# Kernel tuning notes

Hardware: AMD Instinct MI355X
Metric: run time of the kernel (lower is better)

Reference implementation:

```python
import jax, jax.numpy as jnp
import numpy as np

B, S, I, H, O, E, K = 2, 2048, 4096, 1376, 4096, 8, 2
BALANCE_W = 0.01  # balance_loss_weight in llama-moe


def setup_inputs() -> dict:
    key = jax.random.key(0)
    ks = jax.random.split(key, 6)
    sc = lambda k, shape, fan: jax.random.normal(k, shape, jnp.float32) * (fan ** -0.5)
    return {
        "x": jax.random.normal(ks[0], (B, S, I), jnp.float32),
        "gate_w": sc(ks[1], (E, I), I),          # linear gate network, no bias
        "w_gate": sc(ks[2], (E, H, I), I),       # GLU gate proj per expert
        "b_gate": jnp.zeros((E, H), jnp.float32),
        "w_up": sc(ks[3], (E, H, I), I),         # GLU up proj per expert
        "b_up": jnp.zeros((E, H), jnp.float32),
        "w_down": sc(ks[4], (E, O, H), H),       # down proj per expert
        "b_down": jnp.zeros((E, O), jnp.float32),
    }


def _cv_squared(v, eps=1e-10):
    # torch: x.var() / (x.mean()**2 + eps), unbiased variance
    mean = jnp.mean(v)
    var = jnp.sum((v - mean) ** 2) / (v.shape[0] - 1)
    return var / (mean ** 2 + eps)


def reference(x, gate_w, w_gate, b_gate, w_up, b_up, w_down, b_down):
    bsz, seq, _ = x.shape
    xt = x.reshape(-1, I)                         # [T, I] tokens
    T = xt.shape[0]

    # ---- TopKBalancedNoisyGate (no-noise branch) ----
    logits = xt @ gate_w.T                        # [T, E]
    top_logits, top_idx = jax.lax.top_k(logits, K)
    top_scores = jax.nn.softmax(top_logits, axis=-1)   # softmax over top-k logits
    # dense routing matrix: zeros.scatter(1, top_idx, top_scores)
    dense = jnp.zeros((T, E), xt.dtype).at[jnp.arange(T)[:, None], top_idx].set(top_scores)
    importance = dense.sum(axis=0)                # [E]
    load = (dense > 0).astype(jnp.float32).sum(axis=0)  # [E]
    gate_loss = BALANCE_W * (_cv_squared(importance) + _cv_squared(load))

    # ---- UniversalCalculator over LinearGLUExperts ----
    # Dense-dispatch formulation: compute every expert on every token, weight by
    # the (mostly-zero) routing matrix -> identical math to gather/grouped-GEMM/scatter.
    g = jnp.einsum('ti,ehi->teh', xt, w_gate) + b_gate        # [T, E, H]
    u = jnp.einsum('ti,ehi->teh', xt, w_up) + b_up            # [T, E, H]
    inter = jax.nn.silu(g) * u                                # GLU
    # score * (W_down h + b_down) == W_down (score*h) + score*b_down
    y = jnp.einsum('teh,eoh->to', inter * dense[:, :, None], w_down) + dense @ b_down
    return y.reshape(bsz, seq, O), gate_loss
```

## Files before the change

### kernel.cpp

```cpp
#include <hip/hip_runtime.h>
#include <hip/hip_bf16.h>
#include <stdint.h>

#define TN 4096
#define DI 4096
#define DH 1376
#define DHP 1408
#define DO 4096
#define NE 8
#define NPAIR 8192

typedef unsigned short u16;
typedef __bf16 bf16x8 __attribute__((ext_vector_type(8)));
typedef float f32x4 __attribute__((ext_vector_type(4)));
typedef uint32_t u32x4 __attribute__((ext_vector_type(4)));

__device__ __forceinline__ uint32_t pack2bf(float a, float b) {
    union { float f; uint32_t u; } ua, ub;
    ua.f = a; ub.f = b;
    uint32_t lo = (ua.u + 0x7fffu + ((ua.u >> 16) & 1u)) >> 16;
    uint32_t hi = (ub.u + 0x7fffu + ((ub.u >> 16) & 1u)) >> 16;
    return lo | (hi << 16);
}
__device__ __forceinline__ u16 f2bf(float a) {
    union { float f; uint32_t u; } ua; ua.f = a;
    return (u16)((ua.u + 0x7fffu + ((ua.u >> 16) & 1u)) >> 16);
}
__device__ __forceinline__ void gload16(const void* g, void* l) {
    __builtin_amdgcn_global_load_lds(
        (const __attribute__((address_space(1))) void*)g,
        (__attribute__((address_space(3))) void*)l, 16, 0, 0);
}

__global__ __launch_bounds__(256) void k_cvt(const float* __restrict__ src,
                                             u16* __restrict__ dst, int n8)
{
    int i = blockIdx.x * 256 + threadIdx.x;
    if (i >= n8) return;
    const float4* s = (const float4*)(src + (size_t)i * 8);
    float4 a = s[0], b = s[1];
    u32x4 q = {pack2bf(a.x, a.y), pack2bf(a.z, a.w), pack2bf(b.x, b.y), pack2bf(b.z, b.w)};
    *(u32x4*)(dst + (size_t)i * 8) = q;
}

__global__ __launch_bounds__(256) void k_cvt_wd(const float* __restrict__ src,
                                                u16* __restrict__ dst)
{
    int i = blockIdx.x * 256 + threadIdx.x;
    int row = i / 176, c8 = (i % 176) * 8;
    u32x4 q = {0u, 0u, 0u, 0u};
    if (c8 < DH) {
        const float4* s = (const float4*)(src + (size_t)row * DH + c8);
        float4 a = s[0], b = s[1];
        q = (u32x4){pack2bf(a.x, a.y), pack2bf(a.z, a.w), pack2bf(b.x, b.y), pack2bf(b.z, b.w)};
    }
    *(u32x4*)(dst + (size_t)row * DHP + c8) = q;
}

__global__ __launch_bounds__(256) void k_gate(
    const float* __restrict__ x, const float* __restrict__ gw,
    u16* __restrict__ x16, int* __restrict__ tke, float* __restrict__ tks,
    int* __restrict__ cnt, float* __restrict__ imp)
{
    int t = blockIdx.x, tid = threadIdx.x;
    const float* xr = x + (size_t)t * DI;
    double acc[NE];
#pragma unroll
    for (int e = 0; e < NE; ++e) acc[e] = 0.0;
#pragma unroll
    for (int j = 0; j < 4; ++j) {
        int i4 = (j * 256 + tid) * 4;
        float4 xv = *(const float4*)(xr + i4);
        uint2 p; p.x = pack2bf(xv.x, xv.y); p.y = pack2bf(xv.z, xv.w);
        *(uint2*)(x16 + (size_t)t * DI + i4) = p;
#pragma unroll
        for (int e = 0; e < NE; ++e) {
            float4 wv = *(const float4*)(gw + (size_t)e * DI + i4);
            acc[e] = fma((double)xv.x, (double)wv.x, acc[e]);
            acc[e] = fma((double)xv.y, (double)wv.y, acc[e]);
            acc[e] = fma((double)xv.z, (double)wv.z, acc[e]);
            acc[e] = fma((double)xv.w, (double)wv.w, acc[e]);
        }
    }
#pragma unroll
    for (int o = 32; o > 0; o >>= 1)
#pragma unroll
        for (int e = 0; e < NE; ++e) acc[e] += __shfl_down(acc[e], o, 64);
    __shared__ double lred[4][NE];
    if ((tid & 63) == 0)
#pragma unroll
        for (int e = 0; e < NE; ++e) lred[tid >> 6][e] = acc[e];
    __syncthreads();
    if (tid == 0) {
        double lg[NE];
#pragma unroll
        for (int e = 0; e < NE; ++e) lg[e] = lred[0][e] + lred[1][e] + lred[2][e] + lred[3][e];
        int e1 = 0;
        for (int e = 1; e < NE; ++e) if (lg[e] > lg[e1]) e1 = e;
        int e2 = -1;
        for (int e = 0; e < NE; ++e) { if (e == e1) continue; if (e2 < 0 || lg[e] > lg[e2]) e2 = e; }
        float d = (float)(lg[e2] - lg[e1]);
        float ed = expf(d);
        float s1 = 1.0f / (1.0f + ed);
        float s2 = ed / (1.0f + ed);
        tke[2 * t] = e1; tke[2 * t + 1] = e2;
        tks[2 * t] = s1; tks[2 * t + 1] = s2;
        atomicAdd(&cnt[e1], 1); atomicAdd(&cnt[e2], 1);
        unsafeAtomicAdd(&imp[e1], s1); unsafeAtomicAdd(&imp[e2], s2);
    }
}

__global__ void k_finalize(const int* __restrict__ cnt, const float* __restrict__ imp,
                           int* __restrict__ off, float* __restrict__ loss_out)
{
    if (threadIdx.x == 0 && blockIdx.x == 0) {
        int o = 0;
        for (int e = 0; e < NE; ++e) { off[e] = o; o += cnt[e]; }
        float m1 = 0.f, m2 = 0.f;
        for (int e = 0; e < NE; ++e) { m1 += imp[e]; m2 += (float)cnt[e]; }
        m1 *= 0.125f; m2 *= 0.125f;
        float v1 = 0.f, v2 = 0.f;
        for (int e = 0; e < NE; ++e) {
            float d1 = imp[e] - m1, d2 = (float)cnt[e] - m2;
            v1 += d1 * d1; v2 += d2 * d2;
        }
        v1 /= 7.0f; v2 /= 7.0f;
        float cv1 = v1 / (m1 * m1 + 1e-10f);
        float cv2 = v2 / (m2 * m2 + 1e-10f);
        *loss_out = 0.01f * (cv1 + cv2);
    }
}

__global__ __launch_bounds__(256) void k_scatter(
    const int* __restrict__ tke, const float* __restrict__ tks,
    const int* __restrict__ off, int* __restrict__ fill,
    int* __restrict__ tok, float* __restrict__ sc)
{
    int t = blockIdx.x * 256 + threadIdx.x;
    if (t >= TN) return;
#pragma unroll
    for (int k = 0; k < 2; ++k) {
        int e = tke[2 * t + k];
        int pos = off[e] + atomicAdd(&fill[e], 1);
        tok[pos] = t; sc[pos] = tks[2 * t + k];
    }
}

__global__ __launch_bounds__(256) void k_yinit(
    const int* __restrict__ tke, const float* __restrict__ tks,
    const float* __restrict__ bd, float* __restrict__ y)
{
    int t = blockIdx.x, tid = threadIdx.x;
    int e1 = tke[2 * t], e2 = tke[2 * t + 1];
    float s1 = tks[2 * t], s2 = tks[2 * t + 1];
    const float4* b1 = (const float4*)(bd + (size_t)e1 * DO);
    const float4* b2 = (const float4*)(bd + (size_t)e2 * DO);
    float4* yr = (float4*)(y + (size_t)t * DO);
#pragma unroll
    for (int j = 0; j < 4; ++j) {
        int i = j * 256 + tid;
        float4 a = b1[i], b = b2[i], r;
        r.x = s1 * a.x + s2 * b.x; r.y = s1 * a.y + s2 * b.y;
        r.z = s1 * a.z + s2 * b.z; r.w = s1 * a.w + s2 * b.w;
        yr[i] = r;
    }
}


__global__ __launch_bounds__(256, 2) void k_stage1b(
    const u16* __restrict__ x16,
    const u16* __restrict__ wg16, const u16* __restrict__ wu16,
    const float* __restrict__ bg, const float* __restrict__ bu,
    const int* __restrict__ cnt, const int* __restrict__ off,
    const int* __restrict__ tok, const float* __restrict__ sc,
    u16* __restrict__ inter)
{
    int e = blockIdx.x & 7;
    int ce = cnt[e];
    int rows0 = (blockIdx.x >> 3) * 128;
    if (rows0 >= ce) return;
    int oe = off[e];
    int h0 = blockIdx.y * 128;
    int tid = threadIdx.x;

    __shared__ u16 As[128 * 64];
    __shared__ u16 Gs[128 * 64];
    __shared__ u16 Us[128 * 64];

    int swzc = ((tid & 7) ^ ((tid >> 3) & 7)) * 8;
    const u16* abase[4]; const u16* gbase[4]; const u16* ubase[4];
#pragma unroll
    for (int i = 0; i < 4; ++i) {
        int rl = i * 32 + (tid >> 3);
        int rg = oe + min(rows0 + rl, ce - 1);
        abase[i] = x16 + (size_t)tok[rg] * DI + swzc;
        int hr = min(h0 + rl, DH - 1);
        gbase[i] = wg16 + ((size_t)e * DH + hr) * DI + swzc;
        ubase[i] = wu16 + ((size_t)e * DH + hr) * DI + swzc;
    }
    int wid = tid >> 6, lane = tid & 63;

    f32x4 accg[4][4], accu[4][4];
    f32x4 vz = {0.f, 0.f, 0.f, 0.f};
#pragma unroll
    for (int m = 0; m < 4; ++m)
#pragma unroll
        for (int n = 0; n < 4; ++n) { accg[m][n] = vz; accu[m][n] = vz; }

    int wm = wid >> 1, wn = wid & 1;
    int rA = wm * 64 + (lane & 15);
    int rB = wn * 64 + (lane & 15);
    int quarter = lane >> 4;
    int swzr = lane & 7;

    for (int k0 = 0; k0 < DI; k0 += 64) {
#pragma unroll
        for (int i = 0; i < 4; ++i) {
            gload16(abase[i] + k0, &As[i * 2048 + wid * 512]);
            gload16(gbase[i] + k0, &Gs[i * 2048 + wid * 512]);
            gload16(ubase[i] + k0, &Us[i * 2048 + wid * 512]);
        }
        __syncthreads();
#pragma unroll
        for (int kk = 0; kk < 2; ++kk) {
            int cb = ((kk * 4 + quarter) ^ swzr) * 8;
            bf16x8 a[4], g[4], u[4];
#pragma unroll
            for (int m = 0; m < 4; ++m)
                a[m] = *(const bf16x8*)&As[(rA + m * 16) * 64 + cb];
#pragma unroll
            for (int n = 0; n < 4; ++n) {
                g[n] = *(const bf16x8*)&Gs[(rB + n * 16) * 64 + cb];
                u[n] = *(const bf16x8*)&Us[(rB + n * 16) * 64 + cb];
            }
#pragma unroll
            for (int m = 0; m < 4; ++m)
#pragma unroll
                for (int n = 0; n < 4; ++n) {
                    accg[m][n] = __builtin_amdgcn_mfma_f32_16x16x32_bf16(a[m], g[n], accg[m][n], 0, 0, 0);
                    accu[m][n] = __builtin_amdgcn_mfma_f32_16x16x32_bf16(a[m], u[n], accu[m][n], 0, 0, 0);
                }
        }
        __syncthreads();
    }

    int rmax = ce - rows0;
    float bgv[4], buv[4];
    int hc[4]; bool hok[4];
#pragma unroll
    for (int n = 0; n < 4; ++n) {
        hc[n] = h0 + wn * 64 + n * 16 + (lane & 15);
        hok[n] = hc[n] < DH;
        bgv[n] = hok[n] ? bg[e * DH + hc[n]] : 0.f;
        buv[n] = hok[n] ? bu[e * DH + hc[n]] : 0.f;
    }
#pragma unroll
    for (int m = 0; m < 4; ++m) {
#pragma unroll
        for (int r = 0; r < 4; ++r) {
            int rl = wm * 64 + m * 16 + (lane >> 4) * 4 + r;
            if (rl < rmax) {
                int rg = oe + rows0 + rl;
                float s = sc[rg];
                size_t rowb = (size_t)rg * DHP;
#pragma unroll
                for (int n = 0; n < 4; ++n) {
                    float v = 0.f;
                    if (hok[n]) {
                        float gv = accg[m][n][r] + bgv[n];
                        float uv = accu[m][n][r] + buv[n];
                        float sig = 1.0f / (1.0f + __expf(-gv));
                        v = s * gv * sig * uv;
                    }
                    inter[rowb + hc[n]] = f2bf(v);
                }
            }
        }
    }
}

__global__ __launch_bounds__(256, 2) void k_stage2b(
    const u16* __restrict__ inter, const u16* __restrict__ wd16,
    const int* __restrict__ cnt, const int* __restrict__ off,
    const int* __restrict__ tok, float* __restrict__ y)
{
    int e = blockIdx.x & 7;
    int ce = cnt[e];
    int rows0 = (blockIdx.x >> 3) * 128;
    if (rows0 >= ce) return;
    int oe = off[e];
    int o0 = blockIdx.y * 128;
    int tid = threadIdx.x;

    __shared__ u16 As[128 * 64];
    __shared__ u16 Bs[128 * 64];

    int swzc = ((tid & 7) ^ ((tid >> 3) & 7)) * 8;
    const u16* abase[4]; const u16* bbase[4];
#pragma unroll
    for (int i = 0; i < 4; ++i) {
        int rl = i * 32 + (tid >> 3);
        int ar = min(oe + rows0 + rl, NPAIR - 1);
        abase[i] = inter + (size_t)ar * DHP + swzc;
        bbase[i] = wd16 + ((size_t)e * DO + (o0 + rl)) * DHP + swzc;
    }
    int wid = tid >> 6, lane = tid & 63;

    f32x4 acc[4][4];
    f32x4 vz = {0.f, 0.f, 0.f, 0.f};
#pragma unroll
    for (int m = 0; m < 4; ++m)
#pragma unroll
        for (int n = 0; n < 4; ++n) acc[m][n] = vz;

    int wm = wid >> 1, wn = wid & 1;
    int rA = wm * 64 + (lane & 15);
    int rB = wn * 64 + (lane & 15);
    int quarter = lane >> 4;
    int swzr = lane & 7;

    for (int k0 = 0; k0 < DHP; k0 += 64) {
#pragma unroll
        for (int i = 0; i < 4; ++i) {
            gload16(abase[i] + k0, &As[i * 2048 + wid * 512]);
            gload16(bbase[i] + k0, &Bs[i * 2048 + wid * 512]);
        }
        __syncthreads();
#pragma unroll
        for (int kk = 0; kk < 2; ++kk) {
            int cb = ((kk * 4 + quarter) ^ swzr) * 8;
            bf16x8 a[4], b[4];
#pragma unroll
            for (int m = 0; m < 4; ++m)
                a[m] = *(const bf16x8*)&As[(rA + m * 16) * 64 + cb];
#pragma unroll
            for (int n = 0; n < 4; ++n)
                b[n] = *(const bf16x8*)&Bs[(rB + n * 16) * 64 + cb];
#pragma unroll
            for (int m = 0; m < 4; ++m)
#pragma unroll
                for (int n = 0; n < 4; ++n)
                    acc[m][n] = __builtin_amdgcn_mfma_f32_16x16x32_bf16(a[m], b[n], acc[m][n], 0, 0, 0);
        }
        __syncthreads();
    }

    int rmax = ce - rows0;
#pragma unroll
    for (int m = 0; m < 4; ++m) {
#pragma unroll
        for (int r = 0; r < 4; ++r) {
            int rl = wm * 64 + m * 16 + (lane >> 4) * 4 + r;
            if (rl >= rmax) continue;
            int t = tok[oe + rows0 + rl];
            float* yr = y + (size_t)t * DO + o0 + wn * 64 + (lane & 15);
#pragma unroll
            for (int n = 0; n < 4; ++n)
                unsafeAtomicAdd(yr + n * 16, acc[m][n][r]);
        }
    }
}

__global__ __launch_bounds__(256, 2) void k_stage1_f32(
    const u16* __restrict__ x16,
    const float* __restrict__ wg, const float* __restrict__ wu,
    const float* __restrict__ bg, const float* __restrict__ bu,
    const int* __restrict__ cnt, const int* __restrict__ off,
    const int* __restrict__ tok, const float* __restrict__ sc,
    u16* __restrict__ inter)
{
    int e = blockIdx.x >> 5;
    int ce = cnt[e];
    int rows0 = (blockIdx.x & 31) * 128;
    if (rows0 >= ce) return;
    int oe = off[e];
    int h0 = blockIdx.y * 128;
    int tid = threadIdx.x;

    __shared__ u16 As[128 * 64];
    __shared__ u16 Bgs[128 * 64];
    __shared__ u16 Bus[128 * 64];

    const u16* abase[4];
#pragma unroll
    for (int i = 0; i < 4; ++i) {
        int rl = i * 32 + (tid >> 3);
        int rg = oe + min(rows0 + rl, ce - 1);
        abase[i] = x16 + (size_t)tok[rg] * DI + ((tid & 7) * 8);
    }
    int wid = tid >> 6, lane = tid & 63;

    int bn = tid >> 1;
    int bks = (tid & 1) * 32;
    int hrow = h0 + bn;
    bool bval = hrow < DH;
    const float* wgp = wg + ((size_t)e * DH + (bval ? hrow : 0)) * DI + bks;
    const float* wup = wu + ((size_t)e * DH + (bval ? hrow : 0)) * DI + bks;

    f32x4 accg[4][4], accu[4][4];
    f32x4 vz = {0.f, 0.f, 0.f, 0.f};
#pragma unroll
    for (int m = 0; m < 4; ++m)
#pragma unroll
        for (int n = 0; n < 4; ++n) { accg[m][n] = vz; accu[m][n] = vz; }

    int wm = wid >> 1, wn = wid & 1;
    int arow = wm * 64 + (lane & 15);
    int acol = (lane >> 4) * 8;
    int brow = wn * 64 + (lane & 15);

    for (int k0 = 0; k0 < DI; k0 += 64) {
#pragma unroll
        for (int i = 0; i < 4; ++i)
            gload16(abase[i] + k0, &As[i * 2048 + wid * 512]);
        {
            const float* p = wgp + k0;
            uint32_t pk[16];
#pragma unroll
            for (int j = 0; j < 8; ++j) {
                float4 v = bval ? *(const float4*)(p + j * 4) : make_float4(0.f, 0.f, 0.f, 0.f);
                pk[2 * j] = pack2bf(v.x, v.y); pk[2 * j + 1] = pack2bf(v.z, v.w);
            }
            u32x4* dst = (u32x4*)&Bgs[bn * 64 + bks];
#pragma unroll
            for (int j = 0; j < 4; ++j) {
                u32x4 q = {pk[4 * j], pk[4 * j + 1], pk[4 * j + 2], pk[4 * j + 3]};
                dst[j] = q;
            }
        }
        {
            const float* p = wup + k0;
            uint32_t pk[16];
#pragma unroll
            for (int j = 0; j < 8; ++j) {
                float4 v = bval ? *(const float4*)(p + j * 4) : make_float4(0.f, 0.f, 0.f, 0.f);
                pk[2 * j] = pack2bf(v.x, v.y); pk[2 * j + 1] = pack2bf(v.z, v.w);
            }
            u32x4* dst = (u32x4*)&Bus[bn * 64 + bks];
#pragma unroll
            for (int j = 0; j < 4; ++j) {
                u32x4 q = {pk[4 * j], pk[4 * j + 1], pk[4 * j + 2], pk[4 * j + 3]};
                dst[j] = q;
            }
        }
        __syncthreads();
#pragma unroll
        for (int kk = 0; kk < 2; ++kk) {
            bf16x8 a[4], g[4], u[4];
#pragma unroll
            for (int m = 0; m < 4; ++m)
                a[m] = *(const bf16x8*)&As[(arow + m * 16) * 64 + kk * 32 + acol];
#pragma unroll
            for (int n = 0; n < 4; ++n) {
                g[n] = *(const bf16x8*)&Bgs[(brow + n * 16) * 64 + kk * 32 + acol];
                u[n] = *(const bf16x8*)&Bus[(brow + n * 16) * 64 + kk * 32 + acol];
            }
#pragma unroll
            for (int m = 0; m < 4; ++m)
#pragma unroll
                for (int n = 0; n < 4; ++n) {
                    accg[m][n] = __builtin_amdgcn_mfma_f32_16x16x32_bf16(a[m], g[n], accg[m][n], 0, 0, 0);
                    accu[m][n] = __builtin_amdgcn_mfma_f32_16x16x32_bf16(a[m], u[n], accu[m][n], 0, 0, 0);
                }
        }
        __syncthreads();
    }

    int rmax = ce - rows0;
    float bgv[4], buv[4];
    int hcv[4]; bool hok[4];
#pragma unroll
    for (int n = 0; n < 4; ++n) {
        int hcn = h0 + wn * 64 + n * 16 + (lane & 15);
        hok[n] = hcn < DH; hcv[n] = hok[n] ? hcn : 0;
        bgv[n] = bg[e * DH + hcv[n]];
        buv[n] = bu[e * DH + hcv[n]];
    }
#pragma unroll
    for (int m = 0; m < 4; ++m) {
#pragma unroll
        for (int r = 0; r < 4; ++r) {
            int rl = wm * 64 + m * 16 + (lane >> 4) * 4 + r;
            if (rl < rmax) {
                int rg = oe + rows0 + rl;
                float s = sc[rg];
                size_t rowb = (size_t)rg * DH;
#pragma unroll
                for (int n = 0; n < 4; ++n) {
                    if (hok[n]) {
                        float gv = accg[m][n][r] + bgv[n];
                        float uv = accu[m][n][r] + buv[n];
                        float sig = 1.0f / (1.0f + __expf(-gv));
                        inter[rowb + hcv[n]] = f2bf(s * gv * sig * uv);
                    }
                }
            }
        }
    }
}

__global__ __launch_bounds__(256, 2) void k_stage2_f32(
    const u16* __restrict__ inter, const float* __restrict__ wd,
    const int* __restrict__ cnt, const int* __restrict__ off,
    const int* __restrict__ tok, float* __restrict__ y)
{
    int e = blockIdx.x >> 5;
    int ce = cnt[e];
    int rows0 = (blockIdx.x & 31) * 128;
    if (rows0 >= ce) return;
    int oe = off[e];
    int o0 = blockIdx.y * 128;
    int tid = threadIdx.x;

    __shared__ u16 As[128 * 32];
    __shared__ u16 Bs[128 * 32];

    const u16* asrc[2];
#pragma unroll
    for (int i = 0; i < 2; ++i) {
        int rl = i * 64 + (tid >> 2);
        int rg = min(oe + rows0 + rl, NPAIR - 1);
        asrc[i] = inter + (size_t)rg * DH + (tid & 3) * 8;
    }
    int wid = tid >> 6, lane = tid & 63;
    int bn = tid >> 1, bks = (tid & 1) * 16;
    const float* wdp = wd + ((size_t)e * DO + (o0 + bn)) * DH + bks;

    f32x4 acc[4][4];
    f32x4 vz = {0.f, 0.f, 0.f, 0.f};
#pragma unroll
    for (int m = 0; m < 4; ++m)
#pragma unroll
        for (int n = 0; n < 4; ++n) acc[m][n] = vz;

    int wm = wid >> 1, wn = wid & 1;
    int arow = wm * 64 + (lane & 15);
    int acol = (lane >> 4) * 8;
    int brow = wn * 64 + (lane & 15);

    for (int k0 = 0; k0 < DH; k0 += 32) {
#pragma unroll
        for (int i = 0; i < 2; ++i)
            gload16(asrc[i] + k0, &As[i * 2048 + wid * 512]);
        {
            uint32_t pk[8];
#pragma unroll
            for (int j = 0; j < 4; ++j) {
                float4 v = *(const float4*)(wdp + k0 + j * 4);
                pk[2 * j] = pack2bf(v.x, v.y); pk[2 * j + 1] = pack2bf(v.z, v.w);
            }
            u32x4* dst = (u32x4*)&Bs[bn * 32 + bks];
            u32x4 q0 = {pk[0], pk[1], pk[2], pk[3]};
            u32x4 q1 = {pk[4], pk[5], pk[6], pk[7]};
            dst[0] = q0; dst[1] = q1;
        }
        __syncthreads();
        bf16x8 a[4], b[4];
#pragma unroll
        for (int m = 0; m < 4; ++m) a[m] = *(const bf16x8*)&As[(arow + m * 16) * 32 + acol];
#pragma unroll
        for (int n = 0; n < 4; ++n) b[n] = *(const bf16x8*)&Bs[(brow + n * 16) * 32 + acol];
#pragma unroll
        for (int m = 0; m < 4; ++m)
#pragma unroll
            for (int n = 0; n < 4; ++n)
                acc[m][n] = __builtin_amdgcn_mfma_f32_16x16x32_bf16(a[m], b[n], acc[m][n], 0, 0, 0);
        __syncthreads();
    }

    int rmax = ce - rows0;
#pragma unroll
    for (int m = 0; m < 4; ++m) {
#pragma unroll
        for (int r = 0; r < 4; ++r) {
            int rl = wm * 64 + m * 16 + (lane >> 4) * 4 + r;
            if (rl >= rmax) continue;
            int t = tok[oe + rows0 + rl];
            float* yr = y + (size_t)t * DO + o0 + wn * 64 + (lane & 15);
#pragma unroll
            for (int n = 0; n < 4; ++n)
                unsafeAtomicAdd(yr + n * 16, acc[m][n][r]);
        }
    }
}

extern "C" void kernel_launch(void* const* d_in, const int* in_sizes, int n_in,
                              void* d_out, int out_size, void* d_ws, size_t ws_size,
                              hipStream_t stream)
{
    const float* x  = (const float*)d_in[0];
    const float* gw = (const float*)d_in[1];
    const float* wg = (const float*)d_in[2];
    const float* bg = (const float*)d_in[3];
    const float* wu = (const float*)d_in[4];
    const float* bu = (const float*)d_in[5];
    const float* wd = (const float*)d_in[6];
    const float* bd = (const float*)d_in[7];
    float* y = (float*)d_out;
    float* loss = y + (size_t)TN * DO;

    uint8_t* ws = (uint8_t*)d_ws;

    if (ws_size >= 329384064ull) {
        u16*   x16   = (u16*)(ws + 0);
        u16*   inter = (u16*)(ws + 33554432ull);
        u16*   wg16  = (u16*)(ws + 56623104ull);
        u16*   wu16  = (u16*)(ws + 146800640ull);
        u16*   wd16  = (u16*)(ws + 236978176ull);
        int*   tok   = (int*)(ws + 329252864ull);
        float* sc    = (float*)(ws + 329285632ull);
        int*   tke   = (int*)(ws + 329318400ull);
        float* tks   = (float*)(ws + 329351168ull);
        int*   misc  = (int*)(ws + 329383936ull);
        int* cnt = misc; int* fill = misc + 8; int* off = misc + 16;
        float* imp = (float*)(misc + 24);

        hipMemsetAsync(misc, 0, 128, stream);
        k_cvt<<<22016, 256, 0, stream>>>(wg, wg16, 5636096);
        k_cvt<<<22016, 256, 0, stream>>>(wu, wu16, 5636096);
        k_cvt_wd<<<22528, 256, 0, stream>>>(wd, wd16);
        k_gate<<<TN, 256, 0, stream>>>(x, gw, x16, tke, tks, cnt, imp);
        k_finalize<<<1, 64, 0, stream>>>(cnt, imp, off, loss);
        k_scatter<<<TN / 256, 256, 0, stream>>>(tke, tks, off, fill, tok, sc);
        k_yinit<<<TN, 256, 0, stream>>>(tke, tks, bd, y);
        k_stage1b<<<dim3(256, 11), 256, 0, stream>>>(x16, wg16, wu16, bg, bu, cnt, off, tok, sc, inter);
        k_stage2b<<<dim3(256, 32), 256, 0, stream>>>(inter, wd16, cnt, off, tok, y);
    } else {
        u16*   x16   = (u16*)(ws + 0);
        u16*   inter = (u16*)(ws + 33554432ull);
        int*   tok   = (int*)(ws + 56098816ull);
        float* sc    = (float*)(ws + 56131584ull);
        int*   tke   = (int*)(ws + 56164352ull);
        float* tks   = (float*)(ws + 56197120ull);
        int*   misc  = (int*)(ws + 56229888ull);
        int* cnt = misc; int* fill = misc + 8; int* off = misc + 16;
        float* imp = (float*)(misc + 24);

        hipMemsetAsync(misc, 0, 128, stream);
        k_gate<<<TN, 256, 0, stream>>>(x, gw, x16, tke, tks, cnt, imp);
        k_finalize<<<1, 64, 0, stream>>>(cnt, imp, off, loss);
        k_scatter<<<TN / 256, 256, 0, stream>>>(tke, tks, off, fill, tok, sc);
        k_yinit<<<TN, 256, 0, stream>>>(tke, tks, bd, y);
        k_stage1_f32<<<dim3(256, 11), 256, 0, stream>>>(x16, wg, wu, bg, bu, cnt, off, tok, sc, inter);
        k_stage2_f32<<<dim3(256, 32), 256, 0, stream>>>(inter, wd, cnt, off, tok, y);
    }
}
```

Measured before the change: 811.4 us.

## Double-buffer LDS tiles with K=32 steps in expert GEMM kernels

```diff
diff --git a/kernel.cpp b/kernel.cpp
--- a/kernel.cpp
+++ b/kernel.cpp
@@ -167,7 +167,7 @@
 }
 
 
-__global__ __launch_bounds__(256, 2) void k_stage1b(
+__global__ __launch_bounds__(256, 3) void k_stage1c(
     const u16* __restrict__ x16,
     const u16* __restrict__ wg16, const u16* __restrict__ wu16,
     const float* __restrict__ bg, const float* __restrict__ bu,
@@ -183,64 +183,70 @@
     int h0 = blockIdx.y * 128;
     int tid = threadIdx.x;
 
-    __shared__ u16 As[128 * 64];
-    __shared__ u16 Gs[128 * 64];
-    __shared__ u16 Us[128 * 64];
-
-    int swzc = ((tid & 7) ^ ((tid >> 3) & 7)) * 8;
-    const u16* abase[4]; const u16* gbase[4]; const u16* ubase[4];
-#pragma unroll
-    for (int i = 0; i < 4; ++i) {
-        int rl = i * 32 + (tid >> 3);
+    __shared__ u16 As[2][128 * 32];
+    __shared__ u16 Gs[2][128 * 32];
+    __shared__ u16 Us[2][128 * 32];
+
+    int swz = ((tid & 3) ^ ((tid >> 3) & 3)) * 8;
+    const u16* abase[2]; const u16* gbase[2]; const u16* ubase[2];
+#pragma unroll
+    for (int i = 0; i < 2; ++i) {
+        int rl = i * 64 + (tid >> 2);
         int rg = oe + min(rows0 + rl, ce - 1);
-        abase[i] = x16 + (size_t)tok[rg] * DI + swzc;
+        abase[i] = x16 + (size_t)tok[rg] * DI + swz;
         int hr = min(h0 + rl, DH - 1);
-        gbase[i] = wg16 + ((size_t)e * DH + hr) * DI + swzc;
-        ubase[i] = wu16 + ((size_t)e * DH + hr) * DI + swzc;
-    }
+        gbase[i] = wg16 + ((size_t)e * DH + hr) * DI + swz;
+        ubase[i] = wu16 + ((size_t)e * DH + hr) * DI + swz;
+    }
+
     int wid = tid >> 6, lane = tid & 63;
-
-    f32x4 accg[4][4], accu[4][4];
-    f32x4 vz = {0.f, 0.f, 0.f, 0.f};
-#pragma unroll
-    for (int m = 0; m < 4; ++m)
-#pragma unroll
-        for (int n = 0; n < 4; ++n) { accg[m][n] = vz; accu[m][n] = vz; }
-
     int wm = wid >> 1, wn = wid & 1;
     int rA = wm * 64 + (lane & 15);
     int rB = wn * 64 + (lane & 15);
-    int quarter = lane >> 4;
-    int swzr = lane & 7;
-
-    for (int k0 = 0; k0 < DI; k0 += 64) {
-#pragma unroll
-        for (int i = 0; i < 4; ++i) {
-            gload16(abase[i] + k0, &As[i * 2048 + wid * 512]);
-            gload16(gbase[i] + k0, &Gs[i * 2048 + wid * 512]);
-            gload16(ubase[i] + k0, &Us[i * 2048 + wid * 512]);
-        }
-        __syncthreads();
-#pragma unroll
-        for (int kk = 0; kk < 2; ++kk) {
-            int cb = ((kk * 4 + quarter) ^ swzr) * 8;
-            bf16x8 a[4], g[4], u[4];
-#pragma unroll
-            for (int m = 0; m < 4; ++m)
-                a[m] = *(const bf16x8*)&As[(rA + m * 16) * 64 + cb];
+    int colb = (((lane >> 4) ^ ((lane >> 1) & 3)) & 3) * 8;
+
+    f32x4 accg[4][4], accu[4][4];
+    f32x4 vz = {0.f, 0.f, 0.f, 0.f};
+#pragma unroll
+    for (int m = 0; m < 4; ++m)
+#pragma unroll
+        for (int n = 0; n < 4; ++n) { accg[m][n] = vz; accu[m][n] = vz; }
+
+#pragma unroll
+    for (int i = 0; i < 2; ++i) {
+        gload16(abase[i], &As[0][i * 2048 + tid * 8]);
+        gload16(gbase[i], &Gs[0][i * 2048 + tid * 8]);
+        gload16(ubase[i], &Us[0][i * 2048 + tid * 8]);
+    }
+    __syncthreads();
+
+    for (int t = 0; t < DI / 32; ++t) {
+        int cur = t & 1;
+        if (t + 1 < DI / 32) {
+            int k0 = (t + 1) * 32;
+#pragma unroll
+            for (int i = 0; i < 2; ++i) {
+                gload16(abase[i] + k0, &As[cur ^ 1][i * 2048 + tid * 8]);
+                gload16(gbase[i] + k0, &Gs[cur ^ 1][i * 2048 + tid * 8]);
+                gload16(ubase[i] + k0, &Us[cur ^ 1][i * 2048 + tid * 8]);
+            }
+        }
+        bf16x8 a[4], g[4], u[4];
+#pragma unroll
+        for (int m = 0; m < 4; ++m)
+            a[m] = *(const bf16x8*)&As[cur][(rA + m * 16) * 32 + colb];
+#pragma unroll
+        for (int n = 0; n < 4; ++n) {
+            g[n] = *(const bf16x8*)&Gs[cur][(rB + n * 16) * 32 + colb];
+            u[n] = *(const bf16x8*)&Us[cur][(rB + n * 16) * 32 + colb];
+        }
+#pragma unroll
+        for (int m = 0; m < 4; ++m)
 #pragma unroll
             for (int n = 0; n < 4; ++n) {
-                g[n] = *(const bf16x8*)&Gs[(rB + n * 16) * 64 + cb];
-                u[n] = *(const bf16x8*)&Us[(rB + n * 16) * 64 + cb];
-            }
-#pragma unroll
-            for (int m = 0; m < 4; ++m)
-#pragma unroll
-                for (int n = 0; n < 4; ++n) {
-                    accg[m][n] = __builtin_amdgcn_mfma_f32_16x16x32_bf16(a[m], g[n], accg[m][n], 0, 0, 0);
-                    accu[m][n] = __builtin_amdgcn_mfma_f32_16x16x32_bf16(a[m], u[n], accu[m][n], 0, 0, 0);
-                }
-        }
+                accg[m][n] = __builtin_amdgcn_mfma_f32_16x16x32_bf16(a[m], g[n], accg[m][n], 0, 0, 0);
+                accu[m][n] = __builtin_amdgcn_mfma_f32_16x16x32_bf16(a[m], u[n], accu[m][n], 0, 0, 0);
+            }
         __syncthreads();
     }
 
@@ -279,7 +285,7 @@
     }
 }
 
-__global__ __launch_bounds__(256, 2) void k_stage2b(
+__global__ __launch_bounds__(256, 4) void k_stage2c(
     const u16* __restrict__ inter, const u16* __restrict__ wd16,
     const int* __restrict__ cnt, const int* __restrict__ off,
     const int* __restrict__ tok, float* __restrict__ y)
@@ -292,56 +298,61 @@
     int o0 = blockIdx.y * 128;
     int tid = threadIdx.x;
 
-    __shared__ u16 As[128 * 64];
-    __shared__ u16 Bs[128 * 64];
-
-    int swzc = ((tid & 7) ^ ((tid >> 3) & 7)) * 8;
-    const u16* abase[4]; const u16* bbase[4];
-#pragma unroll
-    for (int i = 0; i < 4; ++i) {
-        int rl = i * 32 + (tid >> 3);
+    __shared__ u16 As[2][128 * 32];
+    __shared__ u16 Bs[2][128 * 32];
+
+    int swz = ((tid & 3) ^ ((tid >> 3) & 3)) * 8;
+    const u16* abase[2]; const u16* bbase[2];
+#pragma unroll
+    for (int i = 0; i < 2; ++i) {
+        int rl = i * 64 + (tid >> 2);
         int ar = min(oe + rows0 + rl, NPAIR - 1);
-        abase[i] = inter + (size_t)ar * DHP + swzc;
-        bbase[i] = wd16 + ((size_t)e * DO + (o0 + rl)) * DHP + swzc;
-    }
+        abase[i] = inter + (size_t)ar * DHP + swz;
+        bbase[i] = wd16 + ((size_t)e * DO + (o0 + rl)) * DHP + swz;
+    }
+
     int wid = tid >> 6, lane = tid & 63;
-
-    f32x4 acc[4][4];
-    f32x4 vz = {0.f, 0.f, 0.f, 0.f};
-#pragma unroll
-    for (int m = 0; m < 4; ++m)
-#pragma unroll
-        for (int n = 0; n < 4; ++n) acc[m][n] = vz;
-
     int wm = wid >> 1, wn = wid & 1;
     int rA = wm * 64 + (lane & 15);
     int rB = wn * 64 + (lane & 15);
-    int quarter = lane >> 4;
-    int swzr = lane & 7;
-
-    for (int k0 = 0; k0 < DHP; k0 += 64) {
-#pragma unroll
-        for (int i = 0; i < 4; ++i) {
-            gload16(abase[i] + k0, &As[i * 2048 + wid * 512]);
-            gload16(bbase[i] + k0, &Bs[i * 2048 + wid * 512]);
-        }
-        __syncthreads();
-#pragma unroll
-        for (int kk = 0; kk < 2; ++kk) {
-            int cb = ((kk * 4 + quarter) ^ swzr) * 8;
-            bf16x8 a[4], b[4];
-#pragma unroll
-            for (int m = 0; m < 4; ++m)
-                a[m] = *(const bf16x8*)&As[(rA + m * 16) * 64 + cb];
+    int colb = (((lane >> 4) ^ ((lane >> 1) & 3)) & 3) * 8;
+
+    f32x4 acc[4][4];
+    f32x4 vz = {0.f, 0.f, 0.f, 0.f};
+#pragma unroll
+    for (int m = 0; m < 4; ++m)
+#pragma unroll
+        for (int n = 0; n < 4; ++n) acc[m][n] = vz;
+
+#pragma unroll
+    for (int i = 0; i < 2; ++i) {
+        gload16(abase[i], &As[0][i * 2048 + tid * 8]);
+        gload16(bbase[i], &Bs[0][i * 2048 + tid * 8]);
+    }
+    __syncthreads();
+
+    for (int t = 0; t < DHP / 32; ++t) {
+        int cur = t & 1;
+        if (t + 1 < DHP / 32) {
+            int k0 = (t + 1) * 32;
+#pragma unroll
+            for (int i = 0; i < 2; ++i) {
+                gload16(abase[i] + k0, &As[cur ^ 1][i * 2048 + tid * 8]);
+                gload16(bbase[i] + k0, &Bs[cur ^ 1][i * 2048 + tid * 8]);
+            }
+        }
+        bf16x8 a[4], b[4];
+#pragma unroll
+        for (int m = 0; m < 4; ++m)
+            a[m] = *(const bf16x8*)&As[cur][(rA + m * 16) * 32 + colb];
+#pragma unroll
+        for (int n = 0; n < 4; ++n)
+            b[n] = *(const bf16x8*)&Bs[cur][(rB + n * 16) * 32 + colb];
+#pragma unroll
+        for (int m = 0; m < 4; ++m)
 #pragma unroll
             for (int n = 0; n < 4; ++n)
-                b[n] = *(const bf16x8*)&Bs[(rB + n * 16) * 64 + cb];
-#pragma unroll
-            for (int m = 0; m < 4; ++m)
-#pragma unroll
-                for (int n = 0; n < 4; ++n)
-                    acc[m][n] = __builtin_amdgcn_mfma_f32_16x16x32_bf16(a[m], b[n], acc[m][n], 0, 0, 0);
-        }
+                acc[m][n] = __builtin_amdgcn_mfma_f32_16x16x32_bf16(a[m], b[n], acc[m][n], 0, 0, 0);
         __syncthreads();
     }
 
@@ -623,8 +634,8 @@
         k_finalize<<<1, 64, 0, stream>>>(cnt, imp, off, loss);
         k_scatter<<<TN / 256, 256, 0, stream>>>(tke, tks, off, fill, tok, sc);
         k_yinit<<<TN, 256, 0, stream>>>(tke, tks, bd, y);
-        k_stage1b<<<dim3(256, 11), 256, 0, stream>>>(x16, wg16, wu16, bg, bu, cnt, off, tok, sc, inter);
-        k_stage2b<<<dim3(256, 32), 256, 0, stream>>>(inter, wd16, cnt, off, tok, y);
+        k_stage1c<<<dim3(256, 11), 256, 0, stream>>>(x16, wg16, wu16, bg, bu, cnt, off, tok, sc, inter);
+        k_stage2c<<<dim3(256, 32), 256, 0, stream>>>(inter, wd16, cnt, off, tok, y);
     } else {
         u16*   x16   = (u16*)(ws + 0);
         u16*   inter = (u16*)(ws + 33554432ull);
```

After: 1.240 ms. 52.8% more time.
